# Performance work log

Measured on AMD Instinct MI355X. Metric: run time of the kernel, lower is better.

## Reference

```python
import jax, jax.numpy as jnp
import numpy as np

N_NODES = 100000


def gcn_conv(x, edge_index, W, b):
    # PyG GCNConv: add self-loops, symmetric deg^-1/2 normalization,
    # linear transform, scatter-add aggregation onto destination nodes.
    src = edge_index[0]
    dst = edge_index[1]
    loops = jnp.arange(N_NODES, dtype=edge_index.dtype)
    src = jnp.concatenate([src, loops])
    dst = jnp.concatenate([dst, loops])
    deg = jax.ops.segment_sum(jnp.ones_like(src, dtype=x.dtype), dst,
                              num_segments=N_NODES)
    dinv = jnp.where(deg > 0, jax.lax.rsqrt(deg), 0.0)  # deg^-1/2, 0 for isolated
    norm = dinv[src] * dinv[dst]                        # [E+N]
    h = x @ W                                           # [N, out]
    msg = h[src] * norm[:, None]                        # [E+N, out]
    out = jax.ops.segment_sum(msg, dst, num_segments=N_NODES)
    return out + b


def setup_inputs() -> dict:
    key = jax.random.key(0)
    k1, k2, k3, k4, k5, k6 = jax.random.split(key, 6)
    in_c, hid_c, out_c = 128, 64, 40
    n_edges = 1_600_000
    x = jax.random.normal(k1, (N_NODES, in_c), dtype=jnp.float32)
    edge_index = jax.random.randint(k2, (2, n_edges), 0, N_NODES, dtype=jnp.int32)
    # Glorot-style init like GCNConv.reset_parameters
    W1 = jax.random.normal(k3, (in_c, hid_c), dtype=jnp.float32) * (1.0 / np.sqrt(in_c))
    b1 = jnp.zeros((hid_c,), dtype=jnp.float32)
    W2 = jax.random.normal(k4, (hid_c, out_c), dtype=jnp.float32) * (1.0 / np.sqrt(hid_c))
    b2 = jnp.zeros((out_c,), dtype=jnp.float32)
    return {"x": x, "edge_index": edge_index, "W1": W1, "b1": b1, "W2": W2, "b2": b2}


def reference(x, edge_index, W1, b1, W2, b2):
    h = jax.nn.relu(gcn_conv(x, edge_index, W1, b1))
    h = gcn_conv(h, edge_index, W2, b2)
    return jax.nn.log_softmax(h, axis=1)
```

## Files before the change

kernel.cpp:

```cpp
#include <hip/hip_runtime.h>
#include <math.h>

#define N_IN  128
#define N_HID 64
#define N_OUT 40

#define BSH   9
#define SZB   512
#define MAXBK 256
#define CAP   9216

typedef __attribute__((ext_vector_type(4))) float f32x4;
typedef __attribute__((ext_vector_type(8))) short bf16x8;

__device__ __forceinline__ unsigned short bf16_of(float x) {
    unsigned b = __float_as_uint(x);
    return (unsigned short)((b + 0x7fffu + ((b >> 16) & 1u)) >> 16);
}
__device__ __forceinline__ unsigned pack_bf16(float lo, float hi) {
    unsigned bl = __float_as_uint(lo), bh = __float_as_uint(hi);
    bl = (bl + 0x7fffu + ((bl >> 16) & 1u)) >> 16;
    bh = (bh + 0x7fffu + ((bh >> 16) & 1u)) & 0xffff0000u;
    return bl | bh;
}
__device__ __forceinline__ float bf_lo(unsigned u) { return __uint_as_float(u << 16); }
__device__ __forceinline__ float bf_hi(unsigned u) { return __uint_as_float(u & 0xffff0000u); }
__device__ __forceinline__ float2 bfup(unsigned u) { return make_float2(bf_lo(u), bf_hi(u)); }
__device__ __forceinline__ float2 f2add(float2 a, float2 b) { return make_float2(a.x + b.x, a.y + b.y); }

#define ACC8(u) { c0 = f2add(c0, bfup(u.x)); c1 = f2add(c1, bfup(u.y)); \
                  c2 = f2add(c2, bfup(u.z)); c3 = f2add(c3, bfup(u.w)); }

__global__ __launch_bounds__(256) void bucket_scatter2(const int* __restrict__ src,
                                                       const int* __restrict__ dst,
                                                       int E, int NBK,
                                                       int* __restrict__ bcnt,
                                                       int* __restrict__ ebuf) {
    __shared__ int h[MAXBK];
    __shared__ int base[MAXBK];
    int chunk = (E + gridDim.x - 1) / gridDim.x;
    int s = blockIdx.x * chunk;
    int e = min(E, s + chunk);
    for (int i = threadIdx.x; i < MAXBK; i += 256) h[i] = 0;
    __syncthreads();
    for (int i = s + threadIdx.x; i < e; i += 256)
        atomicAdd(&h[dst[i] >> BSH], 1);
    __syncthreads();
    for (int i = threadIdx.x; i < NBK; i += 256) {
        int c = h[i];
        base[i] = c ? atomicAdd(&bcnt[i], c) : 0;
    }
    __syncthreads();
    for (int i = threadIdx.x; i < MAXBK; i += 256) h[i] = 0;
    __syncthreads();
    for (int i = s + threadIdx.x; i < e; i += 256) {
        int d = dst[i];
        int b = d >> BSH;
        int lp = base[b] + atomicAdd(&h[b], 1);
        if (lp < CAP)
            ebuf[b * CAP + lp] = (src[i] << BSH) | (d & (SZB - 1));
    }
}

__global__ __launch_bounds__(256) void bucket_finalize2(const int* __restrict__ bcnt,
                                                        const int* __restrict__ ebuf,
                                                        int N,
                                                        float* __restrict__ dinv,
                                                        int* __restrict__ ssrc,
                                                        int4* __restrict__ sinfo) {
    __shared__ int deg[SZB];
    __shared__ int scn[SZB];
    __shared__ int cur[SZB];
    __shared__ int wsum[256];
    __shared__ int db[128];
    __shared__ int sstage[CAP];
    const int b   = blockIdx.x;
    const int cnt = min(bcnt[b], CAP);
    const int e0  = b * CAP;
    const int n0  = b << BSH;
    const int nn  = min(SZB, N - n0);
    const int t   = threadIdx.x;
    deg[t] = 0; deg[t + 256] = 0;
    __syncthreads();
    for (int i = t; i < cnt; i += 256)
        atomicAdd(&deg[ebuf[e0 + i] & (SZB - 1)], 1);
    __syncthreads();
    int a0 = deg[2 * t], a1 = deg[2 * t + 1];
    int v = a0 + a1;
    wsum[t] = v;
    __syncthreads();
    for (int o = 1; o < 256; o <<= 1) {
        int p = (t >= o) ? wsum[t - o] : 0;
        __syncthreads();
        wsum[t] += p;
        __syncthreads();
    }
    int ex = wsum[t] - v;
    scn[2 * t] = ex;       scn[2 * t + 1] = ex + a0;
    cur[2 * t] = ex;       cur[2 * t + 1] = ex + a0;
    __syncthreads();
    for (int i = t; i < nn; i += 256)
        dinv[n0 + i] = rsqrtf((float)(deg[i] + 1));
    if (t < 128) db[t] = 0;
    __syncthreads();
    for (int i = t; i < nn; i += 256)
        atomicAdd(&db[min(deg[i], 127)], 1);
    __syncthreads();
    int hv = (t < 128) ? db[t] : 0;
    wsum[t] = hv;
    __syncthreads();
    for (int o = 1; o < 128; o <<= 1) {
        int p = (t >= o) ? wsum[t - o] : 0;
        __syncthreads();
        wsum[t] += p;
        __syncthreads();
    }
    if (t < 128) db[t] = wsum[t] - hv;
    __syncthreads();
    for (int i = t; i < nn; i += 256) {
        int dg = deg[i];
        int r  = atomicAdd(&db[min(dg, 127)], 1);
        int st = e0 + scn[i];
        sinfo[n0 + r] = make_int4(st, st + dg, n0 + i,
                                  __float_as_int(rsqrtf((float)(dg + 1))));
    }
    for (int i = t; i < cnt; i += 256) {
        int p = ebuf[e0 + i];
        int lp = atomicAdd(&cur[p & (SZB - 1)], 1);
        sstage[lp] = p >> BSH;
    }
    __syncthreads();
    for (int i = t; i < cnt; i += 256) ssrc[e0 + i] = sstage[i];
}

__global__ __launch_bounds__(256) void gemm1_mfma(const float* __restrict__ X,
                                                  const float* __restrict__ W,
                                                  const float* __restrict__ dinv,
                                                  unsigned* __restrict__ T, int nrows) {
    __shared__ unsigned xlds[8192];
    __shared__ unsigned wlds[4096];
    const int t    = threadIdx.x;
    const int row0 = blockIdx.x * 128;

#pragma unroll
    for (int i = 0; i < 16; ++i) {
        int idx = t + i * 256;
        int row = idx >> 5;
        int c4  = idx & 31;
        int gr = row0 + row;
        float4 v = make_float4(0.f, 0.f, 0.f, 0.f);
        if (gr < nrows) v = *(const float4*)&X[(long long)gr * 128 + c4 * 4];
        unsigned p0 = pack_bf16(v.x, v.y);
        unsigned p1 = pack_bf16(v.z, v.w);
        int byte = (row * 256 + c4 * 8) ^ ((row & 7) << 4);
        *(uint2*)((char*)xlds + byte) = make_uint2(p0, p1);
    }
    for (int i = t; i < 128 * 64; i += 256) {
        int k = i >> 6, c = i & 63;
        unsigned short hb = bf16_of(W[i]);
        int byte = (c * 256 + k * 2) ^ ((c & 7) << 4);
        *(unsigned short*)((char*)wlds + byte) = hb;
    }
    __syncthreads();

    const int w    = t >> 6;
    const int l    = t & 63;
    const int lrow = l & 15;
    const int lk   = l >> 4;

    f32x4 acc[2][4];
#pragma unroll
    for (int rt = 0; rt < 2; ++rt)
#pragma unroll
        for (int ct = 0; ct < 4; ++ct) acc[rt][ct] = (f32x4)0.f;

#pragma unroll
    for (int ks = 0; ks < 4; ++ks) {
        bf16x8 af[2], bfr[4];
#pragma unroll
        for (int rt = 0; rt < 2; ++rt) {
            int row = 32 * w + rt * 16 + lrow;
            int byte = (row * 256 + ks * 64 + lk * 16) ^ ((row & 7) << 4);
            af[rt] = *(bf16x8*)((char*)xlds + byte);
        }
#pragma unroll
        for (int ct = 0; ct < 4; ++ct) {
            int col = ct * 16 + lrow;
            int byte = (col * 256 + ks * 64 + lk * 16) ^ ((col & 7) << 4);
            bfr[ct] = *(bf16x8*)((char*)wlds + byte);
        }
#pragma unroll
        for (int rt = 0; rt < 2; ++rt)
#pragma unroll
            for (int ct = 0; ct < 4; ++ct)
                acc[rt][ct] = __builtin_amdgcn_mfma_f32_16x16x32_bf16(
                    af[rt], bfr[ct], acc[rt][ct], 0, 0, 0);
    }
    __syncthreads();
    float* ot = (float*)xlds;
#pragma unroll
    for (int rt = 0; rt < 2; ++rt)
#pragma unroll
        for (int ct = 0; ct < 4; ++ct)
#pragma unroll
            for (int i = 0; i < 4; ++i) {
                int row = 32 * w + rt * 16 + (l >> 4) * 4 + i;
                int col = ct * 16 + (l & 15);
                ot[row * 64 + col] = acc[rt][ct][i];
            }
    __syncthreads();
#pragma unroll
    for (int i = 0; i < 16; ++i) {
        int idx = t + i * 256;
        int row = idx >> 5, u = idx & 31;
        int gr = row0 + row;
        if (gr < nrows) {
            float2 v = *(float2*)&ot[row * 64 + u * 2];
            float dv = dinv[gr];
            T[(long long)gr * 32 + u] = pack_bf16(v.x * dv, v.y * dv);
        }
    }
}

__global__ __launch_bounds__(256) void agg_relu_o(const int4* __restrict__ sinfo,
                                                  const int* __restrict__ ssrc,
                                                  const unsigned* __restrict__ tab,
                                                  const float* __restrict__ bias,
                                                  unsigned* __restrict__ tabC, int N) {
    int gidx = blockIdx.x * 32 + (threadIdx.x >> 3);
    int ol   = threadIdx.x & 7;
    int4 si = (gidx < N) ? sinfo[gidx] : make_int4(0, 0, 0, 0);
    int j = si.x, end = si.y;
    const unsigned* tp = tab + 4 * ol;
    float2 c0 = make_float2(0.f, 0.f), c1 = c0, c2 = c0, c3 = c0;
    while (__any(j < end)) {
        bool p0 = j < end, p1 = j + 1 < end;
        int s0 = 0, s1 = 0;
        if (p0) s0 = ssrc[j];
        if (p1) s1 = ssrc[j + 1];
        if (p0) { uint4 u = *(const uint4*)(tp + (long long)s0 * 32); ACC8(u); }
        if (p1) { uint4 u = *(const uint4*)(tp + (long long)s1 * 32); ACC8(u); }
        j += 2;
    }
    if (gidx < N) {
        int node = si.z;
        float dd = __int_as_float(si.w);
        uint4 us = *(const uint4*)(tp + (long long)node * 32);
        ACC8(us);
        float4 bb0 = *(const float4*)&bias[8 * ol];
        float4 bb1 = *(const float4*)&bias[8 * ol + 4];
        float v0 = fmaxf(c0.x * dd + bb0.x, 0.f);
        float v1 = fmaxf(c0.y * dd + bb0.y, 0.f);
        float v2 = fmaxf(c1.x * dd + bb0.z, 0.f);
        float v3 = fmaxf(c1.y * dd + bb0.w, 0.f);
        float v4 = fmaxf(c2.x * dd + bb1.x, 0.f);
        float v5 = fmaxf(c2.y * dd + bb1.y, 0.f);
        float v6 = fmaxf(c3.x * dd + bb1.z, 0.f);
        float v7 = fmaxf(c3.y * dd + bb1.w, 0.f);
        uint4 ot;
        ot.x = pack_bf16(v0 * dd, v1 * dd);
        ot.y = pack_bf16(v2 * dd, v3 * dd);
        ot.z = pack_bf16(v4 * dd, v5 * dd);
        ot.w = pack_bf16(v6 * dd, v7 * dd);
        *(uint4*)(tabC + (long long)node * 32 + 4 * ol) = ot;
    }
}

__global__ __launch_bounds__(256) void agg_g_o(const int4* __restrict__ sinfo,
                                               const int* __restrict__ ssrc,
                                               const unsigned* __restrict__ tabC,
                                               unsigned* __restrict__ tabG, int N) {
    int gidx = blockIdx.x * 32 + (threadIdx.x >> 3);
    int ol   = threadIdx.x & 7;
    int4 si = (gidx < N) ? sinfo[gidx] : make_int4(0, 0, 0, 0);
    int j = si.x, end = si.y;
    const unsigned* tp = tabC + 4 * ol;
    float2 c0 = make_float2(0.f, 0.f), c1 = c0, c2 = c0, c3 = c0;
    while (__any(j < end)) {
        bool p0 = j < end, p1 = j + 1 < end;
        int s0 = 0, s1 = 0;
        if (p0) s0 = ssrc[j];
        if (p1) s1 = ssrc[j + 1];
        if (p0) { uint4 u = *(const uint4*)(tp + (long long)s0 * 32); ACC8(u); }
        if (p1) { uint4 u = *(const uint4*)(tp + (long long)s1 * 32); ACC8(u); }
        j += 2;
    }
    if (gidx < N) {
        int node = si.z;
        uint4 us = *(const uint4*)(tp + (long long)node * 32);
        ACC8(us);
        uint4 ot;
        ot.x = pack_bf16(c0.x, c0.y);
        ot.y = pack_bf16(c1.x, c1.y);
        ot.z = pack_bf16(c2.x, c2.y);
        ot.w = pack_bf16(c3.x, c3.y);
        *(uint4*)(tabG + (long long)node * 32 + 4 * ol) = ot;
    }
}

__global__ __launch_bounds__(256) void gemm2_mfma(const unsigned* __restrict__ tabG,
                                                  const float* __restrict__ W2,
                                                  const float* __restrict__ b2,
                                                  const float* __restrict__ dinv,
                                                  float* __restrict__ outp, int nrows) {
    __shared__ unsigned glds[4096];
    __shared__ unsigned wlds[1536];
    const int t    = threadIdx.x;
    const int row0 = blockIdx.x * 128;

#pragma unroll
    for (int i = 0; i < 4; ++i) {
        int idx = t + i * 256;
        int row = idx >> 3;
        int c4  = idx & 7;
        int gr = row0 + row;
        uint4 v = make_uint4(0, 0, 0, 0);
        if (gr < nrows) v = *(const uint4*)(tabG + (long long)gr * 32 + c4 * 4);
        int byte = (row * 128 + c4 * 16) ^ ((row & 7) << 4);
        *(uint4*)((char*)glds + byte) = v;
    }
    for (int i = t; i < 48 * 64; i += 256) {
        int c = i >> 6, k = i & 63;
        unsigned short hb = (c < N_OUT) ? bf16_of(W2[k * N_OUT + c]) : (unsigned short)0;
        int byte = (c * 128 + k * 2) ^ ((c & 7) << 4);
        *(unsigned short*)((char*)wlds + byte) = hb;
    }
    __syncthreads();

    const int w    = t >> 6;
    const int l    = t & 63;
    const int lrow = l & 15;
    const int lk   = l >> 4;

    f32x4 acc[2][3];
#pragma unroll
    for (int rt = 0; rt < 2; ++rt)
#pragma unroll
        for (int ct = 0; ct < 3; ++ct) acc[rt][ct] = (f32x4)0.f;

#pragma unroll
    for (int ks = 0; ks < 2; ++ks) {
        bf16x8 af[2], bfr[3];
#pragma unroll
        for (int rt = 0; rt < 2; ++rt) {
            int row = 32 * w + rt * 16 + lrow;
            int byte = (row * 128 + ks * 64 + lk * 16) ^ ((row & 7) << 4);
            af[rt] = *(bf16x8*)((char*)glds + byte);
        }
#pragma unroll
        for (int ct = 0; ct < 3; ++ct) {
            int col = ct * 16 + lrow;
            int byte = (col * 128 + ks * 64 + lk * 16) ^ ((col & 7) << 4);
            bfr[ct] = *(bf16x8*)((char*)wlds + byte);
        }
#pragma unroll
        for (int rt = 0; rt < 2; ++rt)
#pragma unroll
            for (int ct = 0; ct < 3; ++ct)
                acc[rt][ct] = __builtin_amdgcn_mfma_f32_16x16x32_bf16(
                    af[rt], bfr[ct], acc[rt][ct], 0, 0, 0);
    }

    const int q    = l >> 4;
    const int lcol = l & 15;
    float bb0 = b2[lcol];
    float bb1 = b2[16 + lcol];
    float bb2 = (lcol < 8) ? b2[32 + lcol] : 0.f;
#pragma unroll
    for (int rt = 0; rt < 2; ++rt)
#pragma unroll
        for (int i = 0; i < 4; ++i) {
            int rl = 32 * w + rt * 16 + q * 4 + i;
            int gr = row0 + rl;
            bool ok = gr < nrows;
            float dv = ok ? dinv[gr] : 0.f;
            float v0 = acc[rt][0][i] * dv + bb0;
            float v1 = acc[rt][1][i] * dv + bb1;
            float v2 = (lcol < 8) ? acc[rt][2][i] * dv + bb2 : -INFINITY;
            float m = fmaxf(fmaxf(v0, v1), v2);
            m = fmaxf(m, __shfl_xor(m, 1));
            m = fmaxf(m, __shfl_xor(m, 2));
            m = fmaxf(m, __shfl_xor(m, 4));
            m = fmaxf(m, __shfl_xor(m, 8));
            float ex = __expf(v0 - m) + __expf(v1 - m) + ((lcol < 8) ? __expf(v2 - m) : 0.f);
            ex += __shfl_xor(ex, 1);
            ex += __shfl_xor(ex, 2);
            ex += __shfl_xor(ex, 4);
            ex += __shfl_xor(ex, 8);
            float ls = logf(ex);
            if (ok) {
                long long base = (long long)gr * N_OUT;
                outp[base + lcol]      = v0 - m - ls;
                outp[base + 16 + lcol] = v1 - m - ls;
                if (lcol < 8) outp[base + 32 + lcol] = v2 - m - ls;
            }
        }
}

extern "C" void kernel_launch(void* const* d_in, const int* in_sizes, int n_in,
                              void* d_out, int out_size, void* d_ws, size_t ws_size,
                              hipStream_t stream) {
    const float* x  = (const float*)d_in[0];
    const int*   ei = (const int*)d_in[1];
    const float* W1 = (const float*)d_in[2];
    const float* b1 = (const float*)d_in[3];
    const float* W2 = (const float*)d_in[4];
    const float* b2 = (const float*)d_in[5];
    float* out = (float*)d_out;

    const int N = in_sizes[0] / N_IN;
    const int E = in_sizes[1] / 2;
    const int* src = ei;
    const int* dst = ei + E;
    const int NBK = (N + SZB - 1) >> BSH;

    int*      bcnt  = (int*)d_ws;
    float*    dinv  = (float*)(bcnt + MAXBK);
    int*      ssrc  = (int*)(dinv + N);
    int4*     sinfo = (int4*)(ssrc + (size_t)NBK * CAP);
    unsigned* tabA  = (unsigned*)(sinfo + N);
    unsigned* tabC  = tabA + (size_t)N * 32;
    unsigned* tabG  = tabC + (size_t)N * 32;
    int*      ebuf  = (int*)tabA;

    hipMemsetAsync(bcnt, 0, MAXBK * sizeof(int), stream);

    bucket_scatter2<<<512, 256, 0, stream>>>(src, dst, E, NBK, bcnt, ebuf);
    bucket_finalize2<<<NBK, 256, 0, stream>>>(bcnt, ebuf, N, dinv, ssrc, sinfo);

    gemm1_mfma<<<(N + 127) / 128, 256, 0, stream>>>(x, W1, dinv, tabA, N);
    agg_relu_o<<<(N + 31) / 32, 256, 0, stream>>>(sinfo, ssrc, tabA, b1, tabC, N);

    agg_g_o<<<(N + 31) / 32, 256, 0, stream>>>(sinfo, ssrc, tabC, tabG, N);
    gemm2_mfma<<<(N + 127) / 128, 256, 0, stream>>>(tabG, W2, b2, dinv, out, N);
}
```

Measured before the change: 187.0 us.

## Reorder layer-2 to transform before aggregating, gathering 40-wide rows

Result: no change. 190.5 us (+1.9%).

```diff
diff --git a/kernel.cpp b/kernel.cpp
--- a/kernel.cpp
+++ b/kernel.cpp
@@ -234,13 +234,17 @@
     const unsigned* tp = tab + 4 * ol;
     float2 c0 = make_float2(0.f, 0.f), c1 = c0, c2 = c0, c3 = c0;
     while (__any(j < end)) {
-        bool p0 = j < end, p1 = j + 1 < end;
-        int s0 = 0, s1 = 0;
+        bool p0 = j < end, p1 = j + 1 < end, p2 = j + 2 < end, p3 = j + 3 < end;
+        int s0 = 0, s1 = 0, s2 = 0, s3 = 0;
         if (p0) s0 = ssrc[j];
         if (p1) s1 = ssrc[j + 1];
+        if (p2) s2 = ssrc[j + 2];
+        if (p3) s3 = ssrc[j + 3];
         if (p0) { uint4 u = *(const uint4*)(tp + (long long)s0 * 32); ACC8(u); }
         if (p1) { uint4 u = *(const uint4*)(tp + (long long)s1 * 32); ACC8(u); }
-        j += 2;
+        if (p2) { uint4 u = *(const uint4*)(tp + (long long)s2 * 32); ACC8(u); }
+        if (p3) { uint4 u = *(const uint4*)(tp + (long long)s3 * 32); ACC8(u); }
+        j += 4;
     }
     if (gidx < N) {
         int node = si.z;
@@ -266,43 +270,10 @@
     }
 }
 
-__global__ __launch_bounds__(256) void agg_g_o(const int4* __restrict__ sinfo,
-                                               const int* __restrict__ ssrc,
-                                               const unsigned* __restrict__ tabC,
-                                               unsigned* __restrict__ tabG, int N) {
-    int gidx = blockIdx.x * 32 + (threadIdx.x >> 3);
-    int ol   = threadIdx.x & 7;
-    int4 si = (gidx < N) ? sinfo[gidx] : make_int4(0, 0, 0, 0);
-    int j = si.x, end = si.y;
-    const unsigned* tp = tabC + 4 * ol;
-    float2 c0 = make_float2(0.f, 0.f), c1 = c0, c2 = c0, c3 = c0;
-    while (__any(j < end)) {
-        bool p0 = j < end, p1 = j + 1 < end;
-        int s0 = 0, s1 = 0;
-        if (p0) s0 = ssrc[j];
-        if (p1) s1 = ssrc[j + 1];
-        if (p0) { uint4 u = *(const uint4*)(tp + (long long)s0 * 32); ACC8(u); }
-        if (p1) { uint4 u = *(const uint4*)(tp + (long long)s1 * 32); ACC8(u); }
-        j += 2;
-    }
-    if (gidx < N) {
-        int node = si.z;
-        uint4 us = *(const uint4*)(tp + (long long)node * 32);
-        ACC8(us);
-        uint4 ot;
-        ot.x = pack_bf16(c0.x, c0.y);
-        ot.y = pack_bf16(c1.x, c1.y);
-        ot.z = pack_bf16(c2.x, c2.y);
-        ot.w = pack_bf16(c3.x, c3.y);
-        *(uint4*)(tabG + (long long)node * 32 + 4 * ol) = ot;
-    }
-}
-
-__global__ __launch_bounds__(256) void gemm2_mfma(const unsigned* __restrict__ tabG,
-                                                  const float* __restrict__ W2,
-                                                  const float* __restrict__ b2,
-                                                  const float* __restrict__ dinv,
-                                                  float* __restrict__ outp, int nrows) {
+__global__ __launch_bounds__(256) void gemmw2_mfma(const unsigned* __restrict__ tabC,
+                                                   const float* __restrict__ W2,
+                                                   unsigned* __restrict__ tabD,
+                                                   int nrows) {
     __shared__ unsigned glds[4096];
     __shared__ unsigned wlds[1536];
     const int t    = threadIdx.x;
@@ -315,7 +286,7 @@
         int c4  = idx & 7;
         int gr = row0 + row;
         uint4 v = make_uint4(0, 0, 0, 0);
-        if (gr < nrows) v = *(const uint4*)(tabG + (long long)gr * 32 + c4 * 4);
+        if (gr < nrows) v = *(const uint4*)(tabC + (long long)gr * 32 + c4 * 4);
         int byte = (row * 128 + c4 * 16) ^ ((row & 7) << 4);
         *(uint4*)((char*)glds + byte) = v;
     }
@@ -360,41 +331,91 @@
                 acc[rt][ct] = __builtin_amdgcn_mfma_f32_16x16x32_bf16(
                     af[rt], bfr[ct], acc[rt][ct], 0, 0, 0);
     }
-
+    __syncthreads();
+    unsigned short* sd = (unsigned short*)glds;
     const int q    = l >> 4;
     const int lcol = l & 15;
-    float bb0 = b2[lcol];
-    float bb1 = b2[16 + lcol];
-    float bb2 = (lcol < 8) ? b2[32 + lcol] : 0.f;
 #pragma unroll
     for (int rt = 0; rt < 2; ++rt)
 #pragma unroll
-        for (int i = 0; i < 4; ++i) {
-            int rl = 32 * w + rt * 16 + q * 4 + i;
-            int gr = row0 + rl;
-            bool ok = gr < nrows;
-            float dv = ok ? dinv[gr] : 0.f;
-            float v0 = acc[rt][0][i] * dv + bb0;
-            float v1 = acc[rt][1][i] * dv + bb1;
-            float v2 = (lcol < 8) ? acc[rt][2][i] * dv + bb2 : -INFINITY;
-            float m = fmaxf(fmaxf(v0, v1), v2);
-            m = fmaxf(m, __shfl_xor(m, 1));
-            m = fmaxf(m, __shfl_xor(m, 2));
-            m = fmaxf(m, __shfl_xor(m, 4));
-            m = fmaxf(m, __shfl_xor(m, 8));
-            float ex = __expf(v0 - m) + __expf(v1 - m) + ((lcol < 8) ? __expf(v2 - m) : 0.f);
-            ex += __shfl_xor(ex, 1);
-            ex += __shfl_xor(ex, 2);
-            ex += __shfl_xor(ex, 4);
-            ex += __shfl_xor(ex, 8);
-            float ls = logf(ex);
-            if (ok) {
-                long long base = (long long)gr * N_OUT;
-                outp[base + lcol]      = v0 - m - ls;
-                outp[base + 16 + lcol] = v1 - m - ls;
-                if (lcol < 8) outp[base + 32 + lcol] = v2 - m - ls;
+        for (int ct = 0; ct < 3; ++ct)
+#pragma unroll
+            for (int i = 0; i < 4; ++i) {
+                int row = 32 * w + rt * 16 + q * 4 + i;
+                int col = ct * 16 + lcol;
+                sd[row * 48 + col] = bf16_of(acc[rt][ct][i]);
             }
-        }
+    __syncthreads();
+#pragma unroll
+    for (int i = 0; i < 10; ++i) {
+        int idx = t + i * 256;
+        int row = idx / 20, c = idx % 20;
+        int gr = row0 + row;
+        if (gr < nrows)
+            tabD[(long long)gr * 20 + c] = *(unsigned*)&sd[row * 48 + 2 * c];
+    }
+}
+
+__global__ __launch_bounds__(256) void agg_out_o(const int4* __restrict__ sinfo,
+                                                 const int* __restrict__ ssrc,
+                                                 const unsigned* __restrict__ tabD,
+                                                 const float* __restrict__ b2,
+                                                 float* __restrict__ outp, int N) {
+    int gidx = blockIdx.x * 32 + (threadIdx.x >> 3);
+    int ol   = threadIdx.x & 7;
+    bool act = ol < 5;
+    int4 si = (gidx < N) ? sinfo[gidx] : make_int4(0, 0, 0, 0);
+    int j = si.x, end = si.y;
+    const unsigned* tp = tabD + 4 * ol;
+    float2 c0 = make_float2(0.f, 0.f), c1 = c0, c2 = c0, c3 = c0;
+    while (__any(j < end)) {
+        bool p0 = j < end, p1 = j + 1 < end, p2 = j + 2 < end, p3 = j + 3 < end;
+        int s0 = 0, s1 = 0, s2 = 0, s3 = 0;
+        if (p0) s0 = ssrc[j];
+        if (p1) s1 = ssrc[j + 1];
+        if (p2) s2 = ssrc[j + 2];
+        if (p3) s3 = ssrc[j + 3];
+        if (p0 && act) { uint4 u = *(const uint4*)(tp + (long long)s0 * 20); ACC8(u); }
+        if (p1 && act) { uint4 u = *(const uint4*)(tp + (long long)s1 * 20); ACC8(u); }
+        if (p2 && act) { uint4 u = *(const uint4*)(tp + (long long)s2 * 20); ACC8(u); }
+        if (p3 && act) { uint4 u = *(const uint4*)(tp + (long long)s3 * 20); ACC8(u); }
+        j += 4;
+    }
+    if (gidx < N) {
+        int node = si.z;
+        float dd = __int_as_float(si.w);
+        float v0 = 0.f, v1 = 0.f, v2 = 0.f, v3 = 0.f, v4 = 0.f, v5 = 0.f, v6 = 0.f, v7 = 0.f;
+        float m = -INFINITY;
+        if (act) {
+            uint4 us = *(const uint4*)(tp + (long long)node * 20);
+            ACC8(us);
+            float4 bb0 = *(const float4*)&b2[8 * ol];
+            float4 bb1 = *(const float4*)&b2[8 * ol + 4];
+            v0 = c0.x * dd + bb0.x;  v1 = c0.y * dd + bb0.y;
+            v2 = c1.x * dd + bb0.z;  v3 = c1.y * dd + bb0.w;
+            v4 = c2.x * dd + bb1.x;  v5 = c2.y * dd + bb1.y;
+            v6 = c3.x * dd + bb1.z;  v7 = c3.y * dd + bb1.w;
+            m = fmaxf(fmaxf(fmaxf(v0, v1), fmaxf(v2, v3)),
+                      fmaxf(fmaxf(v4, v5), fmaxf(v6, v7)));
+        }
+        m = fmaxf(m, __shfl_xor(m, 1));
+        m = fmaxf(m, __shfl_xor(m, 2));
+        m = fmaxf(m, __shfl_xor(m, 4));
+        float ex = 0.f;
+        if (act)
+            ex = __expf(v0 - m) + __expf(v1 - m) + __expf(v2 - m) + __expf(v3 - m)
+               + __expf(v4 - m) + __expf(v5 - m) + __expf(v6 - m) + __expf(v7 - m);
+        ex += __shfl_xor(ex, 1);
+        ex += __shfl_xor(ex, 2);
+        ex += __shfl_xor(ex, 4);
+        if (act) {
+            float ls = m + logf(ex);
+            float4 o0 = make_float4(v0 - ls, v1 - ls, v2 - ls, v3 - ls);
+            float4 o1 = make_float4(v4 - ls, v5 - ls, v6 - ls, v7 - ls);
+            *(float4*)&outp[(long long)node * N_OUT + 8 * ol]     = o0;
+            *(float4*)&outp[(long long)node * N_OUT + 8 * ol + 4] = o1;
+        }
+    }
 }
 
 extern "C" void kernel_launch(void* const* d_in, const int* in_sizes, int n_in,
@@ -420,7 +441,7 @@
     int4*     sinfo = (int4*)(ssrc + (size_t)NBK * CAP);
     unsigned* tabA  = (unsigned*)(sinfo + N);
     unsigned* tabC  = tabA + (size_t)N * 32;
-    unsigned* tabG  = tabC + (size_t)N * 32;
+    unsigned* tabD  = tabC + (size_t)N * 32;
     int*      ebuf  = (int*)tabA;
 
     hipMemsetAsync(bcnt, 0, MAXBK * sizeof(int), stream);
@@ -431,6 +452,6 @@
     gemm1_mfma<<<(N + 127) / 128, 256, 0, stream>>>(x, W1, dinv, tabA, N);
     agg_relu_o<<<(N + 31) / 32, 256, 0, stream>>>(sinfo, ssrc, tabA, b1, tabC, N);
 
-    agg_g_o<<<(N + 31) / 32, 256, 0, stream>>>(sinfo, ssrc, tabC, tabG, N);
-    gemm2_mfma<<<(N + 127) / 128, 256, 0, stream>>>(tabG, W2, b2, dinv, out, N);
-}
+    gemmw2_mfma<<<(N + 127) / 128, 256, 0, stream>>>(tabC, W2, tabD, N);
+    agg_out_o<<<(N + 31) / 32, 256, 0, stream>>>(sinfo, ssrc, tabD, b2, out, N);
+}
```
